# Optimization experiments

Hardware: AMD Instinct MI355X
Metric: run time of the kernel (lower is better)

Reference implementation:

```python
import jax, jax.numpy as jnp
import numpy as np


def setup_inputs() -> dict:
    key = jax.random.key(0)
    k1, k2, k3 = jax.random.split(key, 3)
    N, K, C, M = 16, 32768, 16, 128
    pred_boxes = jax.random.normal(k1, (N, K, 5), dtype=jnp.float32)
    pred_cls = jax.random.normal(k2, (N, K, C), dtype=jnp.float32)
    target = jax.random.uniform(k3, (N, M, 5), dtype=jnp.float32)
    return {"pred_boxes": pred_boxes, "pred_cls": pred_cls, "target": target}


def _losses(pred_boxes, pred_cls, target):
    N, K, _ = pred_boxes.shape
    M = target.shape[1]
    C = pred_cls.shape[2]
    mask = target.sum(axis=2) != 0                      # (N, M)
    maskf = mask.astype(pred_boxes.dtype)
    denom = maskf.sum()
    tboxes = target[..., 1:]                            # (N, M, 4) corners (x1,y1,x2,y2)
    tcls = target[..., 0].astype(jnp.int32)             # (N, M)
    pconf = pred_boxes[..., 4]                          # (N, K)
    pb = pred_boxes[..., :4]                            # (N, K, 4) (x, y, w, h)

    # pred corners (N, 1, K)
    p_x1 = pb[:, None, :, 0]
    p_y1 = pb[:, None, :, 1]
    p_x2 = (pb[..., 2] + pb[..., 0])[:, None, :]
    p_y2 = (pb[..., 3] + pb[..., 1])[:, None, :]
    # target corners (N, M, 1)
    t_x1 = tboxes[..., 0:1]
    t_y1 = tboxes[..., 1:2]
    t_x2 = tboxes[..., 2:3]
    t_y2 = tboxes[..., 3:4]

    ix1 = jnp.maximum(p_x1, t_x1)
    iy1 = jnp.maximum(p_y1, t_y1)
    ix2 = jnp.minimum(p_x2, t_x2)
    iy2 = jnp.minimum(p_y2, t_y2)
    inter = jnp.clip(ix2 - ix1 + 1, 0) * jnp.clip(iy2 - iy1 + 1, 0)   # (N, M, K)
    a1 = (p_x2 - p_x1 + 1) * (p_y2 - p_y1 + 1)
    a2 = (t_x2 - t_x1 + 1) * (t_y2 - t_y1 + 1)
    iou = inter / (a1 + a2 - inter + 1e-16)

    best = jnp.argmax(iou, axis=-1)                     # (N, M)
    best_idx = jnp.where(mask, best, 0)                 # masked targets keep index 0 (as torch init)

    best_pb = jnp.take_along_axis(pb, best_idx[..., None], axis=1)       # (N, M, 4)
    best_cls = jnp.take_along_axis(pred_cls, best_idx[..., None], axis=1)  # (N, M, C)
    # NOTE: faithful to original: conf gather indices are never updated -> always index 0
    conf_idx = jnp.zeros((N, M), dtype=jnp.int32)
    best_conf = jax.nn.sigmoid(jnp.take_along_axis(pconf, conf_idx, axis=1))  # (N, M)

    def masked_mean(v):
        return (v * maskf).sum() / denom

    logp = jax.nn.log_softmax(best_cls, axis=-1)
    ce = -jnp.take_along_axis(logp, tcls[..., None], axis=-1)[..., 0]
    loss_cls = masked_mean(ce)

    loss_x = masked_mean((best_pb[..., 0] - tboxes[..., 0]) ** 2)
    loss_y = masked_mean((best_pb[..., 1] - tboxes[..., 1]) ** 2)
    loss_w = masked_mean((best_pb[..., 2] - (tboxes[..., 2] - tboxes[..., 0])) ** 2)
    loss_h = masked_mean((best_pb[..., 3] - (tboxes[..., 3] - tboxes[..., 1])) ** 2)

    labels = (best_conf > 0.5).astype(best_conf.dtype)
    bce = -(labels * jnp.log(best_conf) + (1.0 - labels) * jnp.log(1.0 - best_conf))
    loss_conf = masked_mean(bce)

    loss = loss_cls + loss_x + loss_y + loss_w + loss_h + loss_conf
    return loss, loss_cls, loss_x, loss_y, loss_w, loss_h, loss_conf


def reference(pred_boxes, pred_cls, target):
    return _losses(pred_boxes, pred_cls, target)
```

## Files before the change

### kernel.cpp

```cpp
#include <hip/hip_runtime.h>
#include <math.h>

constexpr int N_ = 16;
constexpr int K_ = 32768;
constexpr int C_ = 16;
constexpr int M_ = 128;

constexpr int KC = 512;
constexpr int CPB = 2;
constexpr int CPW = K_ / (KC * CPB);
constexpr int WAVES = 8;

#define POISON_U 0xAAAAAAAAu

__device__ __forceinline__ unsigned long long load_agent_u64(
    const unsigned long long* p) {
  return __hip_atomic_load(p, __ATOMIC_RELAXED, __HIP_MEMORY_SCOPE_AGENT);
}
__device__ __forceinline__ void store_agent_u64(unsigned long long* p,
                                                unsigned long long v) {
  __hip_atomic_store(p, v, __ATOMIC_RELAXED, __HIP_MEMORY_SCOPE_AGENT);
}
__device__ __forceinline__ void store_agent_f32(float* p, float v) {
  __hip_atomic_store(p, v, __ATOMIC_RELAXED, __HIP_MEMORY_SCOPE_AGENT);
}
__device__ __forceinline__ float load_agent_f32(const float* p) {
  return __hip_atomic_load(p, __ATOMIC_RELAXED, __HIP_MEMORY_SCOPE_AGENT);
}

__device__ __forceinline__ float vminf_(float a, float b) {
  float r;
  asm("v_min_f32 %0, %1, %2" : "=v"(r) : "v"(a), "v"(b));
  return r;
}
__device__ __forceinline__ float vmaxf_(float a, float b) {
  float r;
  asm("v_max_f32 %0, %1, %2" : "=v"(r) : "v"(a), "v"(b));
  return r;
}
__device__ __forceinline__ float vmax0_(float a) {
  float r;
  asm("v_max_f32 %0, 0, %1" : "=v"(r) : "v"(a));
  return r;
}
__device__ __forceinline__ int vbfi_key_(unsigned mask, unsigned iou_bits,
                                         unsigned idx6) {
  int r;
  asm("v_bfi_b32 %0, %1, %2, %3" : "=v"(r) : "v"(mask), "v"(iou_bits),
      "v"(idx6));
  return r;
}
__device__ __forceinline__ int vmaxi_(int a, int b) {
  int r;
  asm("v_max_i32 %0, %1, %2" : "=v"(r) : "v"(a), "v"(b));
  return r;
}
__device__ __forceinline__ int vmax3i_(int a, int b, int c) {
  int r;
  asm("v_max3_i32 %0, %1, %2, %3" : "=v"(r) : "v"(a), "v"(b), "v"(c));
  return r;
}

__global__ __launch_bounds__(512, 4) void fused_loss_kernel(
    const float* __restrict__ pred_boxes,
    const float* __restrict__ pred_cls,
    const float* __restrict__ target,
    unsigned long long* __restrict__ rowwin,
    float* __restrict__ ws2,
    int* __restrict__ cnt,
    float* __restrict__ out) {
  __shared__ float4 lds4[KC];
  __shared__ float ldsa1[KC];
  __shared__ int key_s[WAVES][CPB][M_];
  __shared__ float red[WAVES][7];
  __shared__ int s_flag;

  const int bx = blockIdx.x;
  const int n = blockIdx.y;
  const int tid = threadIdx.x;

  const int wv = tid >> 6;
  const int lane = tid & 63;
  const int rb = lane & 31;
  const int half = (lane >> 5) & 1;
  const int ks = (wv * 2 + half) * 32;
  const int hbase = ((1 - half) << 5) | 31;

  float tx1[4], ty1[4], tx2[4], ty2[4], a2[4];
#pragma unroll
  for (int j = 0; j < 4; ++j) {
    const float* tg = target + ((size_t)(n * M_ + rb + 32 * j)) * 5;
    tx1[j] = tg[1];
    ty1[j] = tg[2];
    tx2[j] = tg[3] + 1.0f;
    ty2[j] = tg[4] + 1.0f;
    a2[j] = (tg[3] - tg[1] + 1.0f) * (tg[4] - tg[2] + 1.0f) + 1e-16f;
  }

  const unsigned keymask = 0xFFFFFE00u;

  for (int cc = 0; cc < CPB; ++cc) {
    const int k0 = (bx * CPB + cc) * KC;

    {
      const float* p = pred_boxes + ((size_t)(n * K_ + k0 + tid)) * 5;
      const float x = p[0];
      const float y = p[1];
      const float bw = p[2];
      const float bh = p[3];
      const float px2 = bw + x;
      const float py2 = bh + y;
      lds4[tid] = make_float4(x, y, px2 + 1.0f, py2 + 1.0f);
      ldsa1[tid] = (px2 - x + 1.0f) * (py2 - y + 1.0f);
    }
    __syncthreads();

    int best[4];
#pragma unroll
    for (int j = 0; j < 4; ++j) best[j] = (int)0x80000000;

#pragma unroll 4
    for (int kl = 0; kl < 32; kl += 2) {
      const float4 va = lds4[ks + kl];
      const float a1a = ldsa1[ks + kl];
      const float4 vb = lds4[ks + kl + 1];
      const float a1b = ldsa1[ks + kl + 1];
      const unsigned idx6a = (unsigned)(hbase - kl);
      const unsigned idx6b = (unsigned)(hbase - (kl + 1));
#pragma unroll
      for (int j = 0; j < 4; ++j) {
        float wwa = vminf_(va.z, tx2[j]) - vmaxf_(va.x, tx1[j]);
        float hha = vminf_(va.w, ty2[j]) - vmaxf_(va.y, ty1[j]);
        wwa = vmax0_(wwa);
        hha = vmax0_(hha);
        const float intera = wwa * hha;
        const float ioua =
            intera * __builtin_amdgcn_rcpf((a1a + a2[j]) - intera);
        const int keya = vbfi_key_(keymask, __float_as_uint(ioua), idx6a);

        float wwb = vminf_(vb.z, tx2[j]) - vmaxf_(vb.x, tx1[j]);
        float hhb = vminf_(vb.w, ty2[j]) - vmaxf_(vb.y, ty1[j]);
        wwb = vmax0_(wwb);
        hhb = vmax0_(hhb);
        const float interb = wwb * hhb;
        const float ioub =
            interb * __builtin_amdgcn_rcpf((a1b + a2[j]) - interb);
        const int keyb = vbfi_key_(keymask, __float_as_uint(ioub), idx6b);

        best[j] = vmax3i_(best[j], keya, keyb);
      }
    }

#pragma unroll
    for (int j = 0; j < 4; ++j) {
      const int other = __shfl_xor(best[j], 32, 64);
      best[j] = vmaxi_(best[j], other);
    }
    if (lane < 32) {
      const unsigned wvf = (unsigned)(7 - wv) << 6;
#pragma unroll
      for (int j = 0; j < 4; ++j) {
        const unsigned u = (unsigned)best[j];
        key_s[wv][cc][rb + 32 * j] = (int)((u & 0xFFFFFE00u) | wvf | (u & 63u));
      }
    }
    __syncthreads();
  }

  if (tid < M_) {
    unsigned long long bestu = ~0ull;
#pragma unroll
    for (int cc = 0; cc < CPB; ++cc) {
      int mg = vmax3i_(key_s[0][cc][tid], key_s[1][cc][tid], key_s[2][cc][tid]);
      mg = vmax3i_(mg, key_s[3][cc][tid], key_s[4][cc][tid]);
      mg = vmax3i_(mg, key_s[5][cc][tid], key_s[6][cc][tid]);
      mg = vmaxi_(mg, key_s[7][cc][tid]);
      const unsigned e = (unsigned)mg & 511u;
      const int gk = (bx * CPB + cc) * KC + (511 - (int)e);
      const unsigned tr = (unsigned)mg & 0xFFFFFE00u;
      const unsigned ord = tr ^ (unsigned)(((int)tr >> 31) | 0x80000000);
      const unsigned long long u =
          ((unsigned long long)(~ord) << 32) | (unsigned)gk;
      bestu = u < bestu ? u : bestu;
    }
    store_agent_u64(&rowwin[((size_t)n * CPW + bx) * M_ + tid], bestu);
  }

  __syncthreads();
  if (tid == 0) {
    const unsigned old = (unsigned)atomicAdd(&cnt[n], 1);
    s_flag = (old == POISON_U + (CPW - 1)) || (old == CPW - 1);
  }
  __syncthreads();
  if (!s_flag) return;

  {
    const int m = tid & (M_ - 1);
    float acc[7] = {0, 0, 0, 0, 0, 0, 0};
    if (tid < M_) {
      unsigned long long bestk = ~0ull;
#pragma unroll
      for (int g = 0; g < CPW; ++g) {
        const unsigned long long pk =
            load_agent_u64(&rowwin[((size_t)n * CPW + g) * M_ + m]);
        bestk = pk < bestk ? pk : bestk;
      }
      const int bidx0 = (int)(unsigned)bestk;

      const float* tg2 = target + ((size_t)(n * M_ + m)) * 5;
      const float t0 = tg2[0], t1 = tg2[1], t2 = tg2[2], t3 = tg2[3],
                  t4 = tg2[4];
      const float sum5 = t0 + t1 + t2 + t3 + t4;
      const float mk = (sum5 != 0.0f) ? 1.0f : 0.0f;
      const int bidx = (sum5 != 0.0f) ? bidx0 : 0;

      const float* pb = pred_boxes + ((size_t)(n * K_ + bidx)) * 5;
      const float b0 = pb[0], b1 = pb[1], bw = pb[2], bh = pb[3];

      const float4* pc =
          (const float4*)(pred_cls + ((size_t)(n * K_ + bidx)) * C_);
      float vals[C_];
#pragma unroll
      for (int q = 0; q < 4; ++q) {
        const float4 vv = pc[q];
        vals[q * 4 + 0] = vv.x;
        vals[q * 4 + 1] = vv.y;
        vals[q * 4 + 2] = vv.z;
        vals[q * 4 + 3] = vv.w;
      }
      int tcls = (int)t0;
      tcls = tcls < 0 ? 0 : (tcls >= C_ ? C_ - 1 : tcls);
      float mx = -INFINITY;
#pragma unroll
      for (int q = 0; q < C_; ++q) mx = fmaxf(mx, vals[q]);
      float se = 0.0f;
#pragma unroll
      for (int q = 0; q < C_; ++q) se += expf(vals[q] - mx);
      const float ce2 = logf(se) + mx - vals[tcls];

      const float dx = b0 - t1;
      const float dy = b1 - t2;
      const float dw = bw - (t3 - t1);
      const float dh = bh - (t4 - t2);

      const float pcf = pred_boxes[(size_t)n * K_ * 5 + 4];
      const float bc = 1.0f / (1.0f + expf(-pcf));
      const float bce = (bc > 0.5f) ? -logf(bc) : -logf(1.0f - bc);

      acc[0] = mk;
      acc[1] = mk * ce2;
      acc[2] = mk * dx * dx;
      acc[3] = mk * dy * dy;
      acc[4] = mk * dw * dw;
      acc[5] = mk * dh * dh;
      acc[6] = mk * bce;
    }

#pragma unroll
    for (int i = 0; i < 7; ++i) {
      float v = acc[i];
      for (int off = 32; off > 0; off >>= 1) v += __shfl_down(v, off, 64);
      acc[i] = v;
    }
    const int lane2 = tid & 63;
    const int wid = tid >> 6;
    if (lane2 == 0) {
#pragma unroll
      for (int i = 0; i < 7; ++i) red[wid][i] = acc[i];
    }
    __syncthreads();

    if (tid == 0) {
      float sum7[7];
#pragma unroll
      for (int i = 0; i < 7; ++i) {
        float s = 0.0f;
#pragma unroll
        for (int w2 = 0; w2 < WAVES; ++w2) s += red[w2][i];
        sum7[i] = s;
      }
#pragma unroll
      for (int i = 0; i < 7; ++i) store_agent_f32(&ws2[n * 8 + i], sum7[i]);
    }
    __syncthreads();
    if (tid == 0) {
      const unsigned old2 = (unsigned)atomicAdd(&cnt[N_], 1);
      s_flag = (old2 == POISON_U + (N_ - 1)) || (old2 == N_ - 1);
    }
    __syncthreads();
  }

  if (s_flag && tid == 0) {
    float s[7] = {0, 0, 0, 0, 0, 0, 0};
    for (int nn = 0; nn < N_; ++nn)
#pragma unroll
      for (int i = 0; i < 7; ++i) s[i] += load_agent_f32(&ws2[nn * 8 + i]);
    const float denom = s[0];
    const float lc = s[1] / denom;
    const float lx = s[2] / denom;
    const float ly = s[3] / denom;
    const float lw = s[4] / denom;
    const float lh = s[5] / denom;
    const float lf = s[6] / denom;
    out[0] = lc + lx + ly + lw + lh + lf;
    out[1] = lc;
    out[2] = lx;
    out[3] = ly;
    out[4] = lw;
    out[5] = lh;
    out[6] = lf;
  }
}

extern "C" void kernel_launch(void* const* d_in, const int* in_sizes, int n_in,
                              void* d_out, int out_size, void* d_ws, size_t ws_size,
                              hipStream_t stream) {
  const float* pred_boxes = (const float*)d_in[0];
  const float* pred_cls = (const float*)d_in[1];
  const float* target = (const float*)d_in[2];
  float* out = (float*)d_out;

  unsigned long long* rowwin = (unsigned long long*)d_ws;
  float* ws2 = (float*)(rowwin + (size_t)N_ * CPW * M_);
  int* cnt = (int*)(ws2 + N_ * 8);

  dim3 g(CPW, N_);
  fused_loss_kernel<<<g, 512, 0, stream>>>(pred_boxes, pred_cls, target,
                                           rowwin, ws2, cnt, out);
}
```

Baseline: 112.1 us.

## Load prediction boxes directly from global memory with register prefetch instead of LDS

Result: slower. 119.8 us (+6.8%).

```diff
diff --git a/kernel.cpp b/kernel.cpp
--- a/kernel.cpp
+++ b/kernel.cpp
@@ -1,5 +1,6 @@
 #include <hip/hip_runtime.h>
 #include <math.h>
+#include <string.h>
 
 constexpr int N_ = 16;
 constexpr int K_ = 32768;
@@ -59,6 +60,12 @@
   int r;
   asm("v_max3_i32 %0, %1, %2, %3" : "=v"(r) : "v"(a), "v"(b), "v"(c));
   return r;
+}
+
+__device__ __forceinline__ float4 ldb16_(const float* p) {
+  float4 v;
+  __builtin_memcpy(&v, p, 16);
+  return v;
 }
 
 __global__ __launch_bounds__(512, 4) void fused_loss_kernel(
@@ -69,8 +76,6 @@
     float* __restrict__ ws2,
     int* __restrict__ cnt,
     float* __restrict__ out) {
-  __shared__ float4 lds4[KC];
-  __shared__ float ldsa1[KC];
   __shared__ int key_s[WAVES][CPB][M_];
   __shared__ float red[WAVES][7];
   __shared__ int s_flag;
@@ -99,38 +104,41 @@
 
   const unsigned keymask = 0xFFFFFE00u;
 
+#pragma unroll 1
   for (int cc = 0; cc < CPB; ++cc) {
     const int k0 = (bx * CPB + cc) * KC;
-
-    {
-      const float* p = pred_boxes + ((size_t)(n * K_ + k0 + tid)) * 5;
-      const float x = p[0];
-      const float y = p[1];
-      const float bw = p[2];
-      const float bh = p[3];
-      const float px2 = bw + x;
-      const float py2 = bh + y;
-      lds4[tid] = make_float4(x, y, px2 + 1.0f, py2 + 1.0f);
-      ldsa1[tid] = (px2 - x + 1.0f) * (py2 - y + 1.0f);
-    }
-    __syncthreads();
+    const float* pk = pred_boxes + ((size_t)(n * K_ + k0 + ks)) * 5;
 
     int best[4];
 #pragma unroll
     for (int j = 0; j < 4; ++j) best[j] = (int)0x80000000;
 
-#pragma unroll 4
+    float4 ca = ldb16_(pk + 0);
+    float4 cb = ldb16_(pk + 5);
+
+#pragma unroll 2
     for (int kl = 0; kl < 32; kl += 2) {
-      const float4 va = lds4[ks + kl];
-      const float a1a = ldsa1[ks + kl];
-      const float4 vb = lds4[ks + kl + 1];
-      const float a1b = ldsa1[ks + kl + 1];
+      const int nk = (kl + 2) & 31;
+      float4 na = ldb16_(pk + 5 * nk);
+      float4 nb = ldb16_(pk + 5 * (nk + 1));
+
+      const float pxa2 = ca.z + ca.x;
+      const float pya2 = ca.w + ca.y;
+      const float vza = pxa2 + 1.0f;
+      const float vwa = pya2 + 1.0f;
+      const float a1a = (pxa2 - ca.x + 1.0f) * (pya2 - ca.y + 1.0f);
+      const float pxb2 = cb.z + cb.x;
+      const float pyb2 = cb.w + cb.y;
+      const float vzb = pxb2 + 1.0f;
+      const float vwb = pyb2 + 1.0f;
+      const float a1b = (pxb2 - cb.x + 1.0f) * (pyb2 - cb.y + 1.0f);
+
       const unsigned idx6a = (unsigned)(hbase - kl);
       const unsigned idx6b = (unsigned)(hbase - (kl + 1));
 #pragma unroll
       for (int j = 0; j < 4; ++j) {
-        float wwa = vminf_(va.z, tx2[j]) - vmaxf_(va.x, tx1[j]);
-        float hha = vminf_(va.w, ty2[j]) - vmaxf_(va.y, ty1[j]);
+        float wwa = vminf_(vza, tx2[j]) - vmaxf_(ca.x, tx1[j]);
+        float hha = vminf_(vwa, ty2[j]) - vmaxf_(ca.y, ty1[j]);
         wwa = vmax0_(wwa);
         hha = vmax0_(hha);
         const float intera = wwa * hha;
@@ -138,8 +146,8 @@
             intera * __builtin_amdgcn_rcpf((a1a + a2[j]) - intera);
         const int keya = vbfi_key_(keymask, __float_as_uint(ioua), idx6a);
 
-        float wwb = vminf_(vb.z, tx2[j]) - vmaxf_(vb.x, tx1[j]);
-        float hhb = vminf_(vb.w, ty2[j]) - vmaxf_(vb.y, ty1[j]);
+        float wwb = vminf_(vzb, tx2[j]) - vmaxf_(cb.x, tx1[j]);
+        float hhb = vminf_(vwb, ty2[j]) - vmaxf_(cb.y, ty1[j]);
         wwb = vmax0_(wwb);
         hhb = vmax0_(hhb);
         const float interb = wwb * hhb;
@@ -149,6 +157,8 @@
 
         best[j] = vmax3i_(best[j], keya, keyb);
       }
+      ca = na;
+      cb = nb;
     }
 
 #pragma unroll
@@ -164,8 +174,8 @@
         key_s[wv][cc][rb + 32 * j] = (int)((u & 0xFFFFFE00u) | wvf | (u & 63u));
       }
     }
-    __syncthreads();
-  }
+  }
+  __syncthreads();
 
   if (tid < M_) {
     unsigned long long bestu = ~0ull;
@@ -201,9 +211,9 @@
       unsigned long long bestk = ~0ull;
 #pragma unroll
       for (int g = 0; g < CPW; ++g) {
-        const unsigned long long pk =
+        const unsigned long long pk2 =
             load_agent_u64(&rowwin[((size_t)n * CPW + g) * M_ + m]);
-        bestk = pk < bestk ? pk : bestk;
+        bestk = pk2 < bestk ? pk2 : bestk;
       }
       const int bidx0 = (int)(unsigned)bestk;
 
```
